# Kernel tuning notes

Hardware: AMD Instinct MI355X
Metric: run time of the kernel (lower is better)

## Reference

```python
import jax, jax.numpy as jnp
import numpy as np

# Config matching init_kwargs: dim=256, input_resolution=(64,64), num_heads=8,
# stride=2, dynamic_factor=2, window_size=8, Attention_Group=2, postype='rel', k=None
DIM, H, W = 256, 64, 64
HEADS, HG, STRIDE, WS, FACTOR = 8, 2, 2, 8, 2.0
GC = DIM // HG                 # channels per attention group (offset net width)
HC = DIM // HEADS              # per-head channels
RH, RW = H // STRIDE, W // STRIDE
WH, WW = H // WS, W // WS
B = 2
MLP_HID = 4 * DIM
EPS = 1e-5


def _grid_sample(img, grid):
    # img: (N, C, H, W); grid: (N, Hg, Wg, 2) with (row, col) in [-1, 1].
    # Bilinear, align_corners=True, zero padding (matches F.grid_sample).
    N, C, Hi, Wi = img.shape
    rows = (grid[..., 0] + 1.0) * 0.5 * (Hi - 1)
    cols = (grid[..., 1] + 1.0) * 0.5 * (Wi - 1)
    r0f = jnp.floor(rows); c0f = jnp.floor(cols)
    wr = rows - r0f; wc = cols - c0f
    r0 = r0f.astype(jnp.int32); c0 = c0f.astype(jnp.int32)

    def gather(ri, ci):
        valid = ((ri >= 0) & (ri < Hi) & (ci >= 0) & (ci < Wi)).astype(img.dtype)
        rc = jnp.clip(ri, 0, Hi - 1); cc = jnp.clip(ci, 0, Wi - 1)
        vals = jax.vmap(lambda im, r, c: im[:, r, c])(img, rc, cc)  # (N, C, Hg, Wg)
        return vals * valid[:, None]

    return (gather(r0, c0) * ((1 - wr) * (1 - wc))[:, None]
            + gather(r0, c0 + 1) * ((1 - wr) * wc)[:, None]
            + gather(r0 + 1, c0) * (wr * (1 - wc))[:, None]
            + gather(r0 + 1, c0 + 1) * (wr * wc)[:, None])


def _ln2d(z, g, b):
    mu = jnp.mean(z, axis=1, keepdims=True)
    var = jnp.var(z, axis=1, keepdims=True)
    return (z - mu) * jax.lax.rsqrt(var + EPS) * g[None, :, None, None] + b[None, :, None, None]


def _conv1x1(z, w, b=None):
    out = jnp.einsum('oc,bchw->bohw', w, z)
    return out if b is None else out + b[None, :, None, None]


def _forward(x, ln1_g, ln1_b, q_w, q_b, k_w, k_b, v_w, v_b,
             off1_w, off2_w, off3_w, bn_g, bn_b, bn_m, bn_v, off4_w,
             posembed, proj_w, proj_b, ln2_g, ln2_b,
             mlp_w1, mlp_b1, mlp_w2, mlp_b2):
    Bx, C = x.shape[0], x.shape[1]
    R, NW, WT = RH * RW, WH * WW, WS * WS
    scale = C ** -0.5  # original uses dim**-0.5 (not head_dim) as default qk scale

    xa = _ln2d(x, ln1_g, ln1_b)
    q = _conv1x1(xa, q_w, q_b)

    # ---- per-group offset prediction: 3 depthwise strided convs -> BN -> GELU -> 1x1 ----
    qg = q.reshape(Bx * HG, GC, H, W)

    def dw(z, w):
        return jax.lax.conv_general_dilated(z, w, (2, 2), ((1, 1), (1, 1)),
                feature_group_count=GC, dimension_numbers=('NCHW', 'OIHW', 'NCHW'))

    o = dw(dw(dw(qg, off1_w), off2_w), off3_w)  # (B*HG, GC, WH, WW)
    o = (o - bn_m[None, :, None, None]) * jax.lax.rsqrt(bn_v + EPS)[None, :, None, None]
    o = o * bn_g[None, :, None, None] + bn_b[None, :, None, None]
    o = jax.nn.gelu(o, approximate=False)
    off = jnp.einsum('oc,bchw->bohw', off4_w, o)               # (B*HG, 2R, WH, WW)
    off = off.reshape(Bx * HG, 2, R, NW).transpose(0, 3, 2, 1)  # (B*HG, NW, R, 2)
    ranges = jnp.array([1.0 / H, 1.0 / W], dtype=x.dtype)
    off = jnp.tanh(off) * ranges * FACTOR

    # ---- reference points normalized to [-1, 1] (align_corners=True convention) ----
    ref_r = (jnp.arange(RH, dtype=x.dtype) * STRIDE) / (H - 1) * 2.0 - 1.0
    ref_c = (jnp.arange(RW, dtype=x.dtype) * STRIDE) / (W - 1) * 2.0 - 1.0
    ref = jnp.stack(jnp.meshgrid(ref_r, ref_c, indexing='ij'), axis=-1).reshape(R, 2)
    grid = off + ref[None, None]                                # (B*HG, NW, R, 2)

    # ---- deformable gather of values at predicted sample locations ----
    value = xa.reshape(Bx * HG, GC, H, W)
    samp = _grid_sample(value, grid).reshape(Bx, C, NW, R)

    kk = _conv1x1(samp, k_w, k_b).reshape(Bx * HEADS, HC, NW, R).transpose(0, 2, 1, 3)
    vv = _conv1x1(samp, v_w, v_b).reshape(Bx * HEADS, HC, NW, R).transpose(0, 2, 1, 3)

    # ---- windowed queries ----
    wq = q.reshape(Bx * HEADS, HC, H, W).transpose(0, 2, 3, 1)
    wq = wq.reshape(Bx * HEADS, WH, WS, WW, WS, HC).transpose(0, 1, 3, 2, 4, 5)
    wq = wq.reshape(Bx * HEADS, NW, WT, HC) * scale

    attn = jnp.einsum('nwqc,nwcr->nwqr', wq, kk)                # (B*h, NW, WT, R)

    # ---- relative position bias: query pixel vs. (stride-spaced) reference point ----
    rel_y = (jnp.arange(RH) * STRIDE)[None, :] - jnp.arange(H)[:, None] + (H - 1)  # (H, RH)
    rel_x = (jnp.arange(RW) * STRIDE)[None, :] - jnp.arange(W)[:, None] + (W - 1)  # (W, RW)
    t = posembed[:, rel_y, :]                                   # (h, H, RH, 2W-1)
    bias = t[:, :, :, rel_x]                                    # (h, H, RH, W, RW)
    bias = bias.transpose(0, 1, 3, 2, 4).reshape(HEADS, H, W, R)
    bias = bias.reshape(HEADS, WH, WS, WW, WS, R).transpose(0, 1, 3, 2, 4, 5)
    bias = bias.reshape(HEADS, NW, WT, R)

    attn = attn.reshape(Bx, HEADS, NW, WT, R) + bias[None]
    attn = jax.nn.softmax(attn, axis=-1).reshape(Bx * HEADS, NW, WT, R)
    out = jnp.einsum('nwqr,nwcr->nwqc', attn, vv)               # (B*h, NW, WT, HC)
    out = out.reshape(Bx * HEADS, WH, WW, WS, WS, HC).transpose(0, 1, 3, 2, 4, 5)
    out = out.reshape(Bx, HEADS, H, W, HC).transpose(0, 1, 4, 2, 3).reshape(Bx, C, H, W)
    out = _conv1x1(out, proj_w, proj_b)

    x = x + out
    xm = _ln2d(x, ln2_g, ln2_b)
    hdn = jax.nn.gelu(_conv1x1(xm, mlp_w1, mlp_b1), approximate=False)
    return x + _conv1x1(hdn, mlp_w2, mlp_b2)


def setup_inputs() -> dict:
    key = jax.random.key(0)
    ks = jax.random.split(key, 16)
    f32 = jnp.float32

    def n(k, shape, std=0.02):
        return jax.random.normal(k, shape, dtype=f32) * std

    R = RH * RW
    return {
        'x': jax.random.normal(ks[0], (B, DIM, H, W), dtype=f32),
        'ln1_g': jnp.ones((DIM,), f32), 'ln1_b': jnp.zeros((DIM,), f32),
        'q_w': n(ks[1], (DIM, DIM)), 'q_b': jnp.zeros((DIM,), f32),
        'k_w': n(ks[2], (DIM, DIM)), 'k_b': jnp.zeros((DIM,), f32),
        'v_w': n(ks[3], (DIM, DIM)), 'v_b': jnp.zeros((DIM,), f32),
        'off1_w': n(ks[4], (GC, 1, 3, 3)),
        'off2_w': n(ks[5], (GC, 1, 3, 3)),
        'off3_w': n(ks[6], (GC, 1, 3, 3)),
        'bn_g': jnp.ones((GC,), f32), 'bn_b': jnp.zeros((GC,), f32),
        'bn_m': jnp.zeros((GC,), f32), 'bn_v': jnp.ones((GC,), f32),
        'off4_w': n(ks[7], (2 * R, GC)),
        'posembed': n(ks[8], (HEADS, 2 * H - 1, 2 * W - 1), std=0.01),
        'proj_w': n(ks[9], (DIM, DIM)), 'proj_b': jnp.zeros((DIM,), f32),
        'ln2_g': jnp.ones((DIM,), f32), 'ln2_b': jnp.zeros((DIM,), f32),
        'mlp_w1': n(ks[10], (MLP_HID, DIM)), 'mlp_b1': jnp.zeros((MLP_HID,), f32),
        'mlp_w2': n(ks[11], (DIM, MLP_HID)), 'mlp_b2': jnp.zeros((DIM,), f32),
    }


def reference(x, ln1_g, ln1_b, q_w, q_b, k_w, k_b, v_w, v_b,
              off1_w, off2_w, off3_w, bn_g, bn_b, bn_m, bn_v, off4_w,
              posembed, proj_w, proj_b, ln2_g, ln2_b,
              mlp_w1, mlp_b1, mlp_w2, mlp_b2):
    return _forward(x, ln1_g, ln1_b, q_w, q_b, k_w, k_b, v_w, v_b,
                    off1_w, off2_w, off3_w, bn_g, bn_b, bn_m, bn_v, off4_w,
                    posembed, proj_w, proj_b, ln2_g, ln2_b,
                    mlp_w1, mlp_b1, mlp_w2, mlp_b2)
```

## Files before the change

### kernel.cpp

```cpp
#include <hip/hip_runtime.h>
#include <hip/hip_bf16.h>
#include <math.h>


typedef __hip_bfloat16 bf16;
typedef __bf16 bf16x8 __attribute__((ext_vector_type(8)));
typedef float f32x4 __attribute__((ext_vector_type(4)));

union U16x8 { uint4 u4; unsigned short us[8]; };

__device__ __forceinline__ float cvt(float x) { return x; }
__device__ __forceinline__ float cvt(bf16 x) { return __bfloat162float(x); }
__device__ __forceinline__ float b2f(unsigned short u) {
  union { float f; unsigned int v; } x; x.v = ((unsigned int)u) << 16; return x.f;
}
__device__ __forceinline__ unsigned short f2b(float f) {
  bf16 h = __float2bfloat16(f);
  return *reinterpret_cast<unsigned short*>(&h);
}
__device__ __forceinline__ float gelu_f(float x) {
  return 0.5f * x * (1.0f + erff(x * 0.7071067811865475f));
}
__device__ __forceinline__ void stout(float* p, float v) { *p = v; }
__device__ __forceinline__ void stout(bf16* p, float v) { *p = __float2bfloat16(v); }

__global__ __launch_bounds__(256) void prep_kernel(
    const float* __restrict__ q_w, const float* __restrict__ q_b,
    const float* __restrict__ k_w, const float* __restrict__ v_w,
    const float* __restrict__ pjw, const float* __restrict__ w1,
    const float* __restrict__ w2, const float* __restrict__ off4w,
    unsigned short* __restrict__ wqkv, float* __restrict__ bqkv,
    unsigned short* __restrict__ wproj, unsigned short* __restrict__ wmlp1,
    unsigned short* __restrict__ wmlp2, unsigned short* __restrict__ woff4)
{
  int idx = blockIdx.x * 256 + threadIdx.x;
  const int S0 = 1280 * 256;
  const int S1 = S0 + 1280;
  const int S2 = S1 + 256 * 256;
  const int S3 = S2 + 1024 * 256;
  const int S4 = S3 + 256 * 1024;
  const int S5 = S4 + 2048 * 128;
  if (idx < S0) {
    int n = idx >> 8, c = idx & 255;
    float v;
    if (n < 256)       v = q_w[n * 256 + c];
    else if (n < 512)  v = (c < 128)  ? k_w[(n - 256) * 256 + c] : 0.f;
    else if (n < 768)  v = (c >= 128) ? k_w[(n - 512) * 256 + c] : 0.f;
    else if (n < 1024) v = (c < 128)  ? v_w[(n - 768) * 256 + c] : 0.f;
    else               v = (c >= 128) ? v_w[(n - 1024) * 256 + c] : 0.f;
    wqkv[idx] = f2b(v);
  } else if (idx < S1) {
    int n = idx - S0;
    bqkv[n] = (n < 256) ? q_b[n] : 0.f;
  } else if (idx < S2) {
    wproj[idx - S1] = f2b(pjw[idx - S1]);
  } else if (idx < S3) {
    wmlp1[idx - S2] = f2b(w1[idx - S2]);
  } else if (idx < S4) {
    wmlp2[idx - S3] = f2b(w2[idx - S3]);
  } else if (idx < S5) {
    woff4[idx - S4] = f2b(off4w[idx - S4]);
  }
}

__global__ __launch_bounds__(256) void packc_kernel(
    const float* __restrict__ rows_, const float* __restrict__ cols_,
    int* __restrict__ goff, float* __restrict__ gwt)
{
  int idx = blockIdx.x * 256 + threadIdx.x;
  float rowf = rows_[idx], colf = cols_[idx];
  float r0f = floorf(rowf), c0f = floorf(colf);
  float wr = rowf - r0f, wc = colf - c0f;
  int r0 = (int)r0f, c0 = (int)c0f;
  bool rv0 = ((unsigned)r0 < 64u), rv1 = ((unsigned)(r0 + 1) < 64u);
  bool cv0 = ((unsigned)c0 < 64u), cv1 = ((unsigned)(c0 + 1) < 64u);
  float4 w;
  w.x = (rv0 && cv0) ? (1.f - wr) * (1.f - wc) : 0.f;
  w.y = (rv0 && cv1) ? (1.f - wr) * wc : 0.f;
  w.z = (rv1 && cv0) ? wr * (1.f - wc) : 0.f;
  w.w = (rv1 && cv1) ? wr * wc : 0.f;
  goff[idx] = r0 * 64 + c0;
  *(float4*)(gwt + (size_t)idx * 4) = w;
}

__global__ __launch_bounds__(256) void ln1_kernel(
    const float* __restrict__ x, const float* __restrict__ g,
    const float* __restrict__ bta, bf16* __restrict__ out,
    float* __restrict__ xnhwc)
{
  __shared__ float s1[8][32], s2[8][32];
  __shared__ unsigned short tb[32][264];
  int t = threadIdx.x;
  int pos = t & 31, cs = t >> 5;
  int p = blockIdx.x * 32 + pos;
  int bb = p >> 12, hw = p & 4095;
  const float* xp = x + (size_t)bb * 256 * 4096 + hw;
  float vloc[32];
  float sum = 0.f, ss = 0.f;
#pragma unroll
  for (int i = 0; i < 32; ++i) {
    float v = xp[(size_t)(cs * 32 + i) * 4096];
    vloc[i] = v; sum += v; ss += v * v;
  }
  s1[cs][pos] = sum; s2[cs][pos] = ss;
  {
    float* xo = xnhwc + (size_t)p * 256 + cs * 32;
#pragma unroll
    for (int qd = 0; qd < 8; ++qd)
      *(float4*)(xo + qd * 4) = make_float4(vloc[qd*4], vloc[qd*4+1],
                                            vloc[qd*4+2], vloc[qd*4+3]);
  }
  __syncthreads();
  if (cs == 0) {
    float S = 0.f, Q = 0.f;
#pragma unroll
    for (int i = 0; i < 8; ++i) { S += s1[i][pos]; Q += s2[i][pos]; }
    float mu = S * (1.f / 256.f);
    float var = Q * (1.f / 256.f) - mu * mu;
    s1[0][pos] = mu;
    s2[0][pos] = rsqrtf(var + 1e-5f);
  }
  __syncthreads();
  float mu = s1[0][pos], rs = s2[0][pos];
#pragma unroll
  for (int i = 0; i < 32; ++i) {
    int c = cs * 32 + i;
    tb[pos][c] = f2b((vloc[i] - mu) * rs * g[c] + bta[c]);
  }
  __syncthreads();
  int px = t >> 3, grp = t & 7;
  bf16* op = out + ((size_t)blockIdx.x * 32 + px) * 256 + grp * 32;
#pragma unroll
  for (int q = 0; q < 4; ++q)
    *(uint4*)(op + q * 8) = *(const uint4*)&tb[px][grp * 32 + q * 8];
}

__global__ __launch_bounds__(256) void ln2_kernel(
    const bf16* __restrict__ xin, const float* __restrict__ g,
    const float* __restrict__ bta, bf16* __restrict__ out)
{
  __shared__ float sa[8][32], sb[8][32];
  __shared__ float mu_s[32], rs_s[32];
  int t = threadIdx.x;
  int px = t >> 3, grp = t & 7;
  size_t p = (size_t)blockIdx.x * 32 + px;
  const bf16* xp = xin + p * 256 + grp * 32;
  float v[32]; float sum = 0.f, ss = 0.f;
#pragma unroll
  for (int q = 0; q < 4; ++q) {
    U16x8 u; u.u4 = *(const uint4*)(xp + q * 8);
#pragma unroll
    for (int j = 0; j < 8; ++j) {
      float f = b2f(u.us[j]); v[q * 8 + j] = f; sum += f; ss += f * f;
    }
  }
  sa[grp][px] = sum; sb[grp][px] = ss;
  __syncthreads();
  if (t < 32) {
    float S = 0.f, Q = 0.f;
#pragma unroll
    for (int i = 0; i < 8; ++i) { S += sa[i][t]; Q += sb[i][t]; }
    float mu = S * (1.f / 256.f);
    mu_s[t] = mu;
    rs_s[t] = rsqrtf(Q * (1.f / 256.f) - mu * mu + 1e-5f);
  }
  __syncthreads();
  float mu = mu_s[px], rs = rs_s[px];
  bf16* op = out + p * 256 + grp * 32;
#pragma unroll
  for (int q = 0; q < 4; ++q) {
    U16x8 o;
#pragma unroll
    for (int j = 0; j < 8; ++j) {
      int c = grp * 32 + q * 8 + j;
      o.us[j] = f2b((v[q * 8 + j] - mu) * rs * g[c] + bta[c]);
    }
    *(uint4*)(op + q * 8) = o.u4;
  }
}

template<int OUTM, int RESM, int ACT, int BM>
__global__ __launch_bounds__(256) void mgemm_kernel(
    const bf16* __restrict__ A, const unsigned short* __restrict__ Bw,
    const float* __restrict__ bias, const void* __restrict__ res,
    void* __restrict__ out, int N, int K, int lda, int ldb)
{
  constexpr int MT = BM / 32;
// ... 23 lines not shown
      int idx = t + i * 256;
      int m = idx >> 3, oc = (idx & 7) * 8;
      *(uint4*)&As[m][oc] = *(const uint4*)(A + (size_t)(m0 + m) * lda + k0 + oc);
    }
#pragma unroll
    for (int i = 0; i < 2; ++i) {
      int idx = t + i * 256;
      int n = idx >> 3, oc = (idx & 7) * 8;
      *(uint4*)&Bs[n][oc] = *(const uint4*)(Bw + (size_t)(n0 + n) * ldb + k0 + oc);
    }
    __syncthreads();
#pragma unroll
    for (int ks = 0; ks < 2; ++ks) {
      bf16x8 af[MT], bfr[2];
#pragma unroll
      for (int mt = 0; mt < MT; ++mt)
        af[mt] = __builtin_bit_cast(bf16x8,
            *(const uint4*)&As[wm + mt * 16 + l15][ks * 32 + quad * 8]);
#pragma unroll
      for (int nt = 0; nt < 2; ++nt)
        bfr[nt] = __builtin_bit_cast(bf16x8,
            *(const uint4*)&Bs[wn + nt * 16 + l15][ks * 32 + quad * 8]);
#pragma unroll
      for (int mt = 0; mt < MT; ++mt)
#pragma unroll
        for (int nt = 0; nt < 2; ++nt)
          acc[mt][nt] = __builtin_amdgcn_mfma_f32_16x16x32_bf16(
              af[mt], bfr[nt], acc[mt][nt], 0, 0, 0);
    }
    __syncthreads();
  }
  float bv[2];
#pragma unroll
  for (int nt = 0; nt < 2; ++nt)
    bv[nt] = bias ? bias[n0 + wn + nt * 16 + l15] : 0.f;
#pragma unroll
  for (int mt = 0; mt < MT; ++mt) {
#pragma unroll
    for (int nt = 0; nt < 2; ++nt) {
#pragma unroll
      for (int reg = 0; reg < 4; ++reg) {
        int m = m0 + wm + mt * 16 + quad * 4 + reg;
        int n = n0 + wn + nt * 16 + l15;
        float v = acc[mt][nt][reg] + bv[nt];
        if constexpr (ACT == 1) v = gelu_f(v);
        if constexpr (RESM == 1)
          v += ((const float*)res)[(size_t)m * N + n];
        if constexpr (RESM == 2)
          v += b2f(((const unsigned short*)res)[(size_t)m * N + n]);
        if constexpr (OUTM == 0)
          ((unsigned short*)out)[(size_t)m * N + n] = f2b(v);
        if constexpr (OUTM == 1)
          T[(n - n0)][(m - m0)] = v;
        if constexpr (OUTM == 3) {
          float val = tanhf(v) * (2.0f / 64.0f);
          int coord = n >> 10, r = n & 1023;
          int rc = coord ? (r & 31) : (r >> 5);
          float ref = rc * (4.0f / 63.0f) - 1.0f;
          float pix = (val + ref + 1.0f) * 31.5f;
          float* dst = coord ? (float*)res : (float*)out;
          dst[(size_t)m * 1024 + r] = pix;
        }
        if constexpr (OUTM == 4)
          ((unsigned short*)out)[((size_t)(n >> 8) * 8192 + m) * 256 + (n & 255)] = f2b(v);
      }
    }
  }
  if constexpr (OUTM == 1) {
    __syncthreads();
    constexpr int SEGS = BM / 32;
    int units = 64 * SEGS;
    if (t < units) {
      int nl = t / SEGS, seg = t % SEGS;
      int bI = m0 >> 12, hw0 = m0 & 4095;
      float* op = (float*)out + ((size_t)bI * 256 + n0 + nl) * 4096 + hw0 + seg * 32;
#pragma unroll
      for (int k = 0; k < 32; ++k) op[k] = T[nl][seg * 32 + k];
    }
  }
}

template<typename TI, typename TO, int IC>
__global__ __launch_bounds__(256) void dwconv_kernel(
    const TI* __restrict__ in, const float* __restrict__ wgt,
    TO* __restrict__ out, int Hi, int Wi, int Ho, int Wo, int fuse,
    const float* __restrict__ bg_, const float* __restrict__ bb_,
    const float* __restrict__ bm_, const float* __restrict__ bv_)
{
  int idx = blockIdx.x * 256 + threadIdx.x;
  int c = idx & 127;
  int pp = idx >> 7;
  int ow = pp % Wo, oh = (pp / Wo) % Ho, bgi = pp / (Wo * Ho);
  const TI* ip;
  if constexpr (IC == 256)
    ip = in + ((size_t)(bgi >> 1) * 4096) * 256 + (bgi & 1) * 128 + c;
  else
    ip = in + ((size_t)bgi * Hi * Wi) * 128 + c;
  float acc = 0.f;
#pragma unroll
  for (int ky = 0; ky < 3; ++ky) {
    int ih = oh * 2 - 1 + ky;
    if ((unsigned)ih >= (unsigned)Hi) continue;
#pragma unroll
    for (int kx = 0; kx < 3; ++kx) {
      int iw = ow * 2 - 1 + kx;
      if ((unsigned)iw >= (unsigned)Wi) continue;
      acc += wgt[c * 9 + ky * 3 + kx] * cvt(ip[(size_t)(ih * Wi + iw) * IC]);
    }
  }
  if (fuse) {
    acc = (acc - bm_[c]) * rsqrtf(bv_[c] + 1e-5f) * bg_[c] + bb_[c];
    acc = gelu_f(acc);
  }
  stout(out + idx, acc);
}

__device__ __forceinline__ void gather_issue(
    int rc0, int b, int nw, int gr_r, int choff,
    const int* __restrict__ goff, const float* __restrict__ gwt,
    const unsigned short* __restrict__ Kimg, const unsigned short* __restrict__ Vimg,
    uint4* kc, uint4* vc, f32x4* wv)
{
#pragma unroll
  for (int g = 0; g < 2; ++g) {
    size_t cbase = ((size_t)(b * 2 + g) * 64 + nw) * 1024 + rc0 + gr_r;
    int base = goff[cbase];
    wv[g] = *(const f32x4*)(gwt + cbase * 4);
    int o00 = min(max(base, 0), 4095);
    int o01 = min(max(base + 1, 0), 4095);
    int o10 = min(max(base + 64, 0), 4095);
    int o11 = min(max(base + 65, 0), 4095);
    size_t pb = ((size_t)g * 8192 + (size_t)b * 4096) * 256 + choff;
    kc[g * 4 + 0] = *(const uint4*)(Kimg + pb + (size_t)o00 * 256);
    vc[g * 4 + 0] = *(const uint4*)(Vimg + pb + (size_t)o00 * 256);
    kc[g * 4 + 1] = *(const uint4*)(Kimg + pb + (size_t)o01 * 256);
    vc[g * 4 + 1] = *(const uint4*)(Vimg + pb + (size_t)o01 * 256);
    kc[g * 4 + 2] = *(const uint4*)(Kimg + pb + (size_t)o10 * 256);
    vc[g * 4 + 2] = *(const uint4*)(Vimg + pb + (size_t)o10 * 256);
    kc[g * 4 + 3] = *(const uint4*)(Kimg + pb + (size_t)o11 * 256);
    vc[g * 4 + 3] = *(const uint4*)(Vimg + pb + (size_t)o11 * 256);
  }
}

__global__ __launch_bounds__(256) void attn_kernel(
    const bf16* __restrict__ qbuf, const unsigned short* __restrict__ Kimg,
    const unsigned short* __restrict__ Vimg, const int* __restrict__ goff,
    const float* __restrict__ gwt, const float* __restrict__ vbv,
    const float* __restrict__ pe, bf16* __restrict__ aout)
{
  __shared__ unsigned short ks[2][64][40];
  __shared__ unsigned short vs[2][32][72];
  __shared__ unsigned short PsQs[64][72];
  __shared__ unsigned short pesb[70][72];

  int blk = blockIdx.x;
  int b = blk & 1, head = (blk >> 1) & 7, nw = blk >> 4;
  int wh = nw >> 3, ww = nw & 7;
  int t = threadIdx.x;
  int lane = t & 63, w = t >> 6;
  int l15 = lane & 15, quad = lane >> 4;
  int qc0 = head * 32;
  int gr_r = t >> 2, gr_seg = t & 3;
  int choff = qc0 + gr_seg * 8;

  {
    int qt = t >> 2, oct = t & 3;
    int h = wh * 8 + (qt >> 3), wcol = ww * 8 + (qt & 7);
// ... 119 lines not shown
        int row = gr_seg * 8 + j;
        vs[nxt][row][gr_r ^ (((row >> 3) & 3) * 8)] = f2b(aV[j]);
      }
    }
  }
#pragma unroll
  for (int nt2 = 0; nt2 < 2; ++nt2) {
    float vbias = vbv[qc0 + nt2 * 16 + l15];
#pragma unroll
    for (int reg = 0; reg < 4; ++reg) {
      int q = w * 16 + quad * 4 + reg;
      size_t p = (size_t)b * 4096 + (wh * 8 + (q >> 3)) * 64 + ww * 8 + (q & 7);
      aout[p * 256 + qc0 + nt2 * 16 + l15] =
          __float2bfloat16(oacc[nt2][reg] / l[reg] + vbias);
    }
  }
}

extern "C" void kernel_launch(void* const* d_in, const int* in_sizes, int n_in,
                              void* d_out, int out_size, void* d_ws, size_t ws_size,
                              hipStream_t stream) {
  (void)in_sizes; (void)n_in; (void)out_size; (void)ws_size;
  const float* x     = (const float*)d_in[0];
  const float* ln1g  = (const float*)d_in[1];
  const float* ln1b  = (const float*)d_in[2];
  const float* q_w   = (const float*)d_in[3];
  const float* q_b   = (const float*)d_in[4];
  const float* k_w   = (const float*)d_in[5];
  const float* k_b   = (const float*)d_in[6];
  const float* v_w   = (const float*)d_in[7];
  const float* v_b   = (const float*)d_in[8];
  const float* off1w = (const float*)d_in[9];
  const float* off2w = (const float*)d_in[10];
  const float* off3w = (const float*)d_in[11];
  const float* bng   = (const float*)d_in[12];
  const float* bnb   = (const float*)d_in[13];
  const float* bnm   = (const float*)d_in[14];
  const float* bnv   = (const float*)d_in[15];
  const float* off4w = (const float*)d_in[16];
  const float* pe    = (const float*)d_in[17];
  const float* pjw   = (const float*)d_in[18];
  const float* pjb   = (const float*)d_in[19];
  const float* ln2g  = (const float*)d_in[20];
  const float* ln2b  = (const float*)d_in[21];
  const float* w1    = (const float*)d_in[22];
  const float* b1    = (const float*)d_in[23];
  const float* w2    = (const float*)d_in[24];
  const float* b2    = (const float*)d_in[25];
  (void)k_b;
  float* outp = (float*)d_out;

  char* W = (char*)d_ws;
  bf16*  xa    = (bf16*) (W + 0);
  float* dw1   = (float*)(W + 8388608);
  float* dw2   = (float*)(W + 10485760);
  bf16*  dw3b  = (bf16*) (W + 11010048);
  float* rows  = (float*)(W + 11141120);
  float* cols  = (float*)(W + 12189696);
  bf16*  qkv   = (bf16*) (W + 13238272);
  bf16*  qb    = qkv;
  bf16*  Kimg  = qkv + 2097152;
  bf16*  Vimg  = qkv + 3 * 2097152;
  bf16*  x2    = (bf16*) (W + 34209792);
  float* xnhwc = (float*)(W + 38404096);
  unsigned short* wqkv  = (unsigned short*)(W + 46792704);
  float*          bqkv  = (float*)         (W + 47448064);
  unsigned short* wproj = (unsigned short*)(W + 47453184);
  unsigned short* wmlp1 = (unsigned short*)(W + 47584256);
  unsigned short* wmlp2 = (unsigned short*)(W + 48108544);
  unsigned short* woff4 = (unsigned short*)(W + 48632832);
  int*   goff  = (int*)  (W + 49157120);
  float* gwt   = (float*)(W + 50205696);
  bf16*  aout = xa;
  bf16*  xm   = xa;
  bf16*  hdn  = Kimg;

  prep_kernel<<<4613, 256, 0, stream>>>(q_w, q_b, k_w, v_w, pjw, w1, w2, off4w,
                                        wqkv, bqkv, wproj, wmlp1, wmlp2, woff4);
  ln1_kernel<<<256, 256, 0, stream>>>(x, ln1g, ln1b, xa, xnhwc);
  mgemm_kernel<4, 0, 0, 128><<<dim3(20, 64), 256, 0, stream>>>(
      xa, wqkv, bqkv, nullptr, qkv, 1280, 256, 256, 256);
  dwconv_kernel<bf16, float, 256><<<2048, 256, 0, stream>>>(
      qb, off1w, dw1, 64, 64, 32, 32, 0, nullptr, nullptr, nullptr, nullptr);
  dwconv_kernel<float, float, 128><<<512, 256, 0, stream>>>(
      dw1, off2w, dw2, 32, 32, 16, 16, 0, nullptr, nullptr, nullptr, nullptr);
  dwconv_kernel<float, bf16, 128><<<128, 256, 0, stream>>>(
      dw2, off3w, dw3b, 16, 16, 8, 8, 1, bng, bnb, bnm, bnv);
  mgemm_kernel<3, 0, 0, 128><<<dim3(32, 2), 256, 0, stream>>>(
      dw3b, woff4, nullptr, (const void*)cols, rows, 2048, 128, 128, 128);
  packc_kernel<<<1024, 256, 0, stream>>>(rows, cols, goff, gwt);
  attn_kernel<<<1024, 256, 0, stream>>>(
      qb, (const unsigned short*)Kimg, (const unsigned short*)Vimg,
      goff, gwt, v_b, pe, aout);
  mgemm_kernel<0, 1, 0, 64><<<dim3(4, 128), 256, 0, stream>>>(
      aout, wproj, pjb, (const void*)xnhwc, x2, 256, 256, 256, 256);
  ln2_kernel<<<256, 256, 0, stream>>>(x2, ln2g, ln2b, xm);
  mgemm_kernel<0, 0, 1, 128><<<dim3(16, 64), 256, 0, stream>>>(
      xm, wmlp1, b1, nullptr, hdn, 1024, 256, 256, 256);
  mgemm_kernel<1, 2, 0, 64><<<dim3(4, 128), 256, 0, stream>>>(
      hdn, wmlp2, b2, (const void*)x2, outp, 256, 1024, 1024, 1024);
}
```

Baseline: 316.2 us.

## Fuse dwconv chain, merge LN1 with weight prep, fold sampling-coefficient packing into GEMM

Merges the LN1 kernel and the weight-conversion kernel into one launch. Replaces the three strided depthwise conv launches with a single kernel that keeps the intermediates in shared memory, so the float intermediate buffers are no longer written and read back. Interleaves the offset-projection weight rows so row and column offsets sit in adjacent lanes, letting the GEMM epilogue compute bilinear indices and weights directly and dropping the separate packing kernel. The fused conv runs only 64 blocks with serial loops, which lowers parallelism in exchange for fewer launches and less memory traffic.

```diff
diff --git a/kernel.cpp b/kernel.cpp
--- a/kernel.cpp
+++ b/kernel.cpp
@@ -21,118 +21,98 @@
 __device__ __forceinline__ float gelu_f(float x) {
   return 0.5f * x * (1.0f + erff(x * 0.7071067811865475f));
 }
-__device__ __forceinline__ void stout(float* p, float v) { *p = v; }
-__device__ __forceinline__ void stout(bf16* p, float v) { *p = __float2bfloat16(v); }
-
-__global__ __launch_bounds__(256) void prep_kernel(
+
+__global__ __launch_bounds__(256) void setup_kernel(
+    const float* __restrict__ x, const float* __restrict__ g,
+    const float* __restrict__ bta,
     const float* __restrict__ q_w, const float* __restrict__ q_b,
     const float* __restrict__ k_w, const float* __restrict__ v_w,
     const float* __restrict__ pjw, const float* __restrict__ w1,
     const float* __restrict__ w2, const float* __restrict__ off4w,
+    bf16* __restrict__ out, float* __restrict__ xnhwc,
     unsigned short* __restrict__ wqkv, float* __restrict__ bqkv,
     unsigned short* __restrict__ wproj, unsigned short* __restrict__ wmlp1,
-    unsigned short* __restrict__ wmlp2, unsigned short* __restrict__ woff4)
-{
-  int idx = blockIdx.x * 256 + threadIdx.x;
-  const int S0 = 1280 * 256;
-  const int S1 = S0 + 1280;
-  const int S2 = S1 + 256 * 256;
-  const int S3 = S2 + 1024 * 256;
-  const int S4 = S3 + 256 * 1024;
-  const int S5 = S4 + 2048 * 128;
-  if (idx < S0) {
-    int n = idx >> 8, c = idx & 255;
-    float v;
-    if (n < 256)       v = q_w[n * 256 + c];
-    else if (n < 512)  v = (c < 128)  ? k_w[(n - 256) * 256 + c] : 0.f;
-    else if (n < 768)  v = (c >= 128) ? k_w[(n - 512) * 256 + c] : 0.f;
-    else if (n < 1024) v = (c < 128)  ? v_w[(n - 768) * 256 + c] : 0.f;
-    else               v = (c >= 128) ? v_w[(n - 1024) * 256 + c] : 0.f;
-    wqkv[idx] = f2b(v);
-  } else if (idx < S1) {
-    int n = idx - S0;
-    bqkv[n] = (n < 256) ? q_b[n] : 0.f;
-  } else if (idx < S2) {
-    wproj[idx - S1] = f2b(pjw[idx - S1]);
-  } else if (idx < S3) {
-    wmlp1[idx - S2] = f2b(w1[idx - S2]);
-  } else if (idx < S4) {
-    wmlp2[idx - S3] = f2b(w2[idx - S3]);
-  } else if (idx < S5) {
-    woff4[idx - S4] = f2b(off4w[idx - S4]);
-  }
-}
-
-__global__ __launch_bounds__(256) void packc_kernel(
-    const float* __restrict__ rows_, const float* __restrict__ cols_,
-    int* __restrict__ goff, float* __restrict__ gwt)
-{
-  int idx = blockIdx.x * 256 + threadIdx.x;
-  float rowf = rows_[idx], colf = cols_[idx];
-  float r0f = floorf(rowf), c0f = floorf(colf);
-  float wr = rowf - r0f, wc = colf - c0f;
-  int r0 = (int)r0f, c0 = (int)c0f;
-  bool rv0 = ((unsigned)r0 < 64u), rv1 = ((unsigned)(r0 + 1) < 64u);
-  bool cv0 = ((unsigned)c0 < 64u), cv1 = ((unsigned)(c0 + 1) < 64u);
-  float4 w;
-  w.x = (rv0 && cv0) ? (1.f - wr) * (1.f - wc) : 0.f;
-  w.y = (rv0 && cv1) ? (1.f - wr) * wc : 0.f;
-  w.z = (rv1 && cv0) ? wr * (1.f - wc) : 0.f;
-  w.w = (rv1 && cv1) ? wr * wc : 0.f;
-  goff[idx] = r0 * 64 + c0;
-  *(float4*)(gwt + (size_t)idx * 4) = w;
-}
-
-__global__ __launch_bounds__(256) void ln1_kernel(
-    const float* __restrict__ x, const float* __restrict__ g,
-    const float* __restrict__ bta, bf16* __restrict__ out,
-    float* __restrict__ xnhwc)
+    unsigned short* __restrict__ wmlp2, unsigned short* __restrict__ woff4i)
 {
   __shared__ float s1[8][32], s2[8][32];
   __shared__ unsigned short tb[32][264];
+  int bid = blockIdx.x;
   int t = threadIdx.x;
-  int pos = t & 31, cs = t >> 5;
-  int p = blockIdx.x * 32 + pos;
-  int bb = p >> 12, hw = p & 4095;
-  const float* xp = x + (size_t)bb * 256 * 4096 + hw;
-  float vloc[32];
-  float sum = 0.f, ss = 0.f;
-#pragma unroll
-  for (int i = 0; i < 32; ++i) {
-    float v = xp[(size_t)(cs * 32 + i) * 4096];
-    vloc[i] = v; sum += v; ss += v * v;
-  }
-  s1[cs][pos] = sum; s2[cs][pos] = ss;
-  {
-    float* xo = xnhwc + (size_t)p * 256 + cs * 32;
-#pragma unroll
-    for (int qd = 0; qd < 8; ++qd)
-      *(float4*)(xo + qd * 4) = make_float4(vloc[qd*4], vloc[qd*4+1],
-                                            vloc[qd*4+2], vloc[qd*4+3]);
-  }
-  __syncthreads();
-  if (cs == 0) {
-    float S = 0.f, Q = 0.f;
-#pragma unroll
-    for (int i = 0; i < 8; ++i) { S += s1[i][pos]; Q += s2[i][pos]; }
-    float mu = S * (1.f / 256.f);
-    float var = Q * (1.f / 256.f) - mu * mu;
-    s1[0][pos] = mu;
-    s2[0][pos] = rsqrtf(var + 1e-5f);
-  }
-  __syncthreads();
-  float mu = s1[0][pos], rs = s2[0][pos];
-#pragma unroll
-  for (int i = 0; i < 32; ++i) {
-    int c = cs * 32 + i;
-    tb[pos][c] = f2b((vloc[i] - mu) * rs * g[c] + bta[c]);
-  }
-  __syncthreads();
-  int px = t >> 3, grp = t & 7;
-  bf16* op = out + ((size_t)blockIdx.x * 32 + px) * 256 + grp * 32;
-#pragma unroll
-  for (int q = 0; q < 4; ++q)
-    *(uint4*)(op + q * 8) = *(const uint4*)&tb[px][grp * 32 + q * 8];
+  if (bid < 256) {
+    int pos = t & 31, cs = t >> 5;
+    int p = bid * 32 + pos;
+    int bb = p >> 12, hw = p & 4095;
+    const float* xp = x + (size_t)bb * 256 * 4096 + hw;
+    float vloc[32];
+    float sum = 0.f, ss = 0.f;
+#pragma unroll
+    for (int i = 0; i < 32; ++i) {
+      float v = xp[(size_t)(cs * 32 + i) * 4096];
+      vloc[i] = v; sum += v; ss += v * v;
+    }
+    s1[cs][pos] = sum; s2[cs][pos] = ss;
+    {
+      float* xo = xnhwc + (size_t)p * 256 + cs * 32;
+#pragma unroll
+      for (int qd = 0; qd < 8; ++qd)
+        *(float4*)(xo + qd * 4) = make_float4(vloc[qd*4], vloc[qd*4+1],
+                                              vloc[qd*4+2], vloc[qd*4+3]);
+    }
+    __syncthreads();
+    if (cs == 0) {
+      float S = 0.f, Q = 0.f;
+#pragma unroll
+      for (int i = 0; i < 8; ++i) { S += s1[i][pos]; Q += s2[i][pos]; }
+      float mu = S * (1.f / 256.f);
+      float var = Q * (1.f / 256.f) - mu * mu;
+      s1[0][pos] = mu;
+      s2[0][pos] = rsqrtf(var + 1e-5f);
+    }
+    __syncthreads();
+    float mu = s1[0][pos], rs = s2[0][pos];
+#pragma unroll
+    for (int i = 0; i < 32; ++i) {
+      int c = cs * 32 + i;
+      tb[pos][c] = f2b((vloc[i] - mu) * rs * g[c] + bta[c]);
+    }
+    __syncthreads();
+    int px = t >> 3, grp = t & 7;
+    bf16* op = out + ((size_t)bid * 32 + px) * 256 + grp * 32;
+#pragma unroll
+    for (int q = 0; q < 4; ++q)
+      *(uint4*)(op + q * 8) = *(const uint4*)&tb[px][grp * 32 + q * 8];
+  } else {
+    int idx = (bid - 256) * 256 + t;
+    const int S0 = 1280 * 256;
+    const int S1 = S0 + 1280;
+    const int S2 = S1 + 256 * 256;
+    const int S3 = S2 + 1024 * 256;
+    const int S4 = S3 + 256 * 1024;
+    const int S5 = S4 + 2048 * 128;
+    if (idx < S0) {
+      int n = idx >> 8, c = idx & 255;
+      float v;
+      if (n < 256)       v = q_w[n * 256 + c];
+      else if (n < 512)  v = (c < 128)  ? k_w[(n - 256) * 256 + c] : 0.f;
+      else if (n < 768)  v = (c >= 128) ? k_w[(n - 512) * 256 + c] : 0.f;
+      else if (n < 1024) v = (c < 128)  ? v_w[(n - 768) * 256 + c] : 0.f;
+      else               v = (c >= 128) ? v_w[(n - 1024) * 256 + c] : 0.f;
+      wqkv[idx] = f2b(v);
+    } else if (idx < S1) {
+      int n = idx - S0;
+      bqkv[n] = (n < 256) ? q_b[n] : 0.f;
+    } else if (idx < S2) {
+      wproj[idx - S1] = f2b(pjw[idx - S1]);
+    } else if (idx < S3) {
+      wmlp1[idx - S2] = f2b(w1[idx - S2]);
+    } else if (idx < S4) {
+      wmlp2[idx - S3] = f2b(w2[idx - S3]);
+    } else if (idx < S5) {
+      int kk = idx - S4;
+      int n = kk >> 7, c = kk & 127;
+      woff4i[kk] = f2b(off4w[((size_t)((n & 1) * 1024 + (n >> 1))) * 128 + c]);
+    }
+  }
 }
 
 __global__ __launch_bounds__(256) void ln2_kernel(
@@ -262,17 +242,31 @@
           ((unsigned short*)out)[(size_t)m * N + n] = f2b(v);
         if constexpr (OUTM == 1)
           T[(n - n0)][(m - m0)] = v;
-        if constexpr (OUTM == 3) {
+        if constexpr (OUTM == 4)
+          ((unsigned short*)out)[((size_t)(n >> 8) * 8192 + m) * 256 + (n & 255)] = f2b(v);
+        if constexpr (OUTM == 5) {
           float val = tanhf(v) * (2.0f / 64.0f);
-          int coord = n >> 10, r = n & 1023;
+          int r = n >> 1, coord = n & 1;
           int rc = coord ? (r & 31) : (r >> 5);
           float ref = rc * (4.0f / 63.0f) - 1.0f;
           float pix = (val + ref + 1.0f) * 31.5f;
-          float* dst = coord ? (float*)res : (float*)out;
-          dst[(size_t)m * 1024 + r] = pix;
+          float other = __shfl_xor(pix, 1, 64);
+          if (coord == 0) {
+            float rowp = pix, colp = other;
+            float r0f = floorf(rowp), c0f = floorf(colp);
+            float wr = rowp - r0f, wc = colp - c0f;
+            int r0 = (int)r0f, c0 = (int)c0f;
+            bool rv0 = ((unsigned)r0 < 64u), rv1 = ((unsigned)(r0 + 1) < 64u);
+            bool cv0 = ((unsigned)c0 < 64u), cv1 = ((unsigned)(c0 + 1) < 64u);
+            float4 w4;
+            w4.x = (rv0 && cv0) ? (1.f - wr) * (1.f - wc) : 0.f;
+            w4.y = (rv0 && cv1) ? (1.f - wr) * wc : 0.f;
+            w4.z = (rv1 && cv0) ? wr * (1.f - wc) : 0.f;
+            w4.w = (rv1 && cv1) ? wr * wc : 0.f;
+            ((int*)out)[(size_t)m * 1024 + r] = r0 * 64 + c0;
+            *(float4*)((float*)res + ((size_t)m * 1024 + r) * 4) = w4;
+          }
         }
-        if constexpr (OUTM == 4)
-          ((unsigned short*)out)[((size_t)(n >> 8) * 8192 + m) * 256 + (n & 255)] = f2b(v);
       }
     }
   }
@@ -290,39 +284,87 @@
   }
 }
 
-template<typename TI, typename TO, int IC>
-__global__ __launch_bounds__(256) void dwconv_kernel(
-    const TI* __restrict__ in, const float* __restrict__ wgt,
-    TO* __restrict__ out, int Hi, int Wi, int Ho, int Wo, int fuse,
-    const float* __restrict__ bg_, const float* __restrict__ bb_,
-    const float* __restrict__ bm_, const float* __restrict__ bv_)
+__global__ __launch_bounds__(256) void dwfused_kernel(
+    const bf16* __restrict__ qb, const float* __restrict__ w1_,
+    const float* __restrict__ w2_, const float* __restrict__ w3_,
+    const float* __restrict__ bng, const float* __restrict__ bnb,
+    const float* __restrict__ bnm, const float* __restrict__ bnv,
+    bf16* __restrict__ dw3b)
 {
-  int idx = blockIdx.x * 256 + threadIdx.x;
-  int c = idx & 127;
-  int pp = idx >> 7;
-  int ow = pp % Wo, oh = (pp / Wo) % Ho, bgi = pp / (Wo * Ho);
-  const TI* ip;
-  if constexpr (IC == 256)
-    ip = in + ((size_t)(bgi >> 1) * 4096) * 256 + (bgi & 1) * 128 + c;
-  else
-    ip = in + ((size_t)bgi * Hi * Wi) * 128 + c;
-  float acc = 0.f;
-#pragma unroll
-  for (int ky = 0; ky < 3; ++ky) {
-    int ih = oh * 2 - 1 + ky;
-    if ((unsigned)ih >= (unsigned)Hi) continue;
-#pragma unroll
-    for (int kx = 0; kx < 3; ++kx) {
-      int iw = ow * 2 - 1 + kx;
-      if ((unsigned)iw >= (unsigned)Wi) continue;
-      acc += wgt[c * 9 + ky * 3 + kx] * cvt(ip[(size_t)(ih * Wi + iw) * IC]);
-    }
-  }
-  if (fuse) {
-    acc = (acc - bm_[c]) * rsqrtf(bv_[c] + 1e-5f) * bg_[c] + bb_[c];
+  __shared__ float L1[1024][8];
+  __shared__ float L2[256][8];
+  int blk = blockIdx.x;
+  int bg = blk >> 4, cg = blk & 15;
+  int b = bg >> 1, g = bg & 1;
+  int t = threadIdx.x;
+  int cl = t & 7;
+  int c127 = cg * 8 + cl;
+  int choff = g * 128 + c127;
+  float wreg[9];
+#pragma unroll
+  for (int k = 0; k < 9; ++k) wreg[k] = w1_[c127 * 9 + k];
+  for (int i = 0; i < 32; ++i) {
+    int sp = (t >> 3) + i * 32;
+    int oh = sp >> 5, ow = sp & 31;
+    float acc = 0.f;
+#pragma unroll
+    for (int ky = 0; ky < 3; ++ky) {
+      int ih = oh * 2 - 1 + ky;
+      if ((unsigned)ih >= 64u) continue;
+#pragma unroll
+      for (int kx = 0; kx < 3; ++kx) {
+        int iw = ow * 2 - 1 + kx;
+        if ((unsigned)iw >= 64u) continue;
+        acc += wreg[ky * 3 + kx] *
+               cvt(qb[((size_t)b * 4096 + ih * 64 + iw) * 256 + choff]);
+      }
+    }
+    L1[sp][cl] = acc;
+  }
+  __syncthreads();
+#pragma unroll
+  for (int k = 0; k < 9; ++k) wreg[k] = w2_[c127 * 9 + k];
+  for (int i = 0; i < 8; ++i) {
+    int sp = (t >> 3) + i * 32;
+    int oh = sp >> 4, ow = sp & 15;
+    float acc = 0.f;
+#pragma unroll
+    for (int ky = 0; ky < 3; ++ky) {
+      int ih = oh * 2 - 1 + ky;
+      if ((unsigned)ih >= 32u) continue;
+#pragma unroll
+      for (int kx = 0; kx < 3; ++kx) {
+        int iw = ow * 2 - 1 + kx;
+        if ((unsigned)iw >= 32u) continue;
+        acc += wreg[ky * 3 + kx] * L1[ih * 32 + iw][cl];
+      }
+    }
+    L2[sp][cl] = acc;
+  }
+  __syncthreads();
+#pragma unroll
+  for (int k = 0; k < 9; ++k) wreg[k] = w3_[c127 * 9 + k];
+  float sc = rsqrtf(bnv[c127] + 1e-5f) * bng[c127];
+  float mb = bnm[c127], bb2 = bnb[c127];
+  for (int i = 0; i < 2; ++i) {
+    int sp = (t >> 3) + i * 32;
+    int oh = sp >> 3, ow = sp & 7;
+    float acc = 0.f;
+#pragma unroll
+    for (int ky = 0; ky < 3; ++ky) {
+      int ih = oh * 2 - 1 + ky;
+      if ((unsigned)ih >= 16u) continue;
+#pragma unroll
+      for (int kx = 0; kx < 3; ++kx) {
+        int iw = ow * 2 - 1 + kx;
+        if ((unsigned)iw >= 16u) continue;
+        acc += wreg[ky * 3 + kx] * L2[ih * 16 + iw][cl];
+      }
+    }
+    acc = (acc - mb) * sc + bb2;
     acc = gelu_f(acc);
-  }
-  stout(out + idx, acc);
+    dw3b[((size_t)bg * 64 + sp) * 128 + c127] = __float2bfloat16(acc);
+  }
 }
 
 __device__ __forceinline__ void gather_issue(
@@ -548,43 +590,34 @@
 
   char* W = (char*)d_ws;
   bf16*  xa    = (bf16*) (W + 0);
-  float* dw1   = (float*)(W + 8388608);
-  float* dw2   = (float*)(W + 10485760);
   bf16*  dw3b  = (bf16*) (W + 11010048);
-  float* rows  = (float*)(W + 11141120);
-  float* cols  = (float*)(W + 12189696);
   bf16*  qkv   = (bf16*) (W + 13238272);
   bf16*  qb    = qkv;
   bf16*  Kimg  = qkv + 2097152;
   bf16*  Vimg  = qkv + 3 * 2097152;
   bf16*  x2    = (bf16*) (W + 34209792);
   float* xnhwc = (float*)(W + 38404096);
-  unsigned short* wqkv  = (unsigned short*)(W + 46792704);
-  float*          bqkv  = (float*)         (W + 47448064);
-  unsigned short* wproj = (unsigned short*)(W + 47453184);
-  unsigned short* wmlp1 = (unsigned short*)(W + 47584256);
-  unsigned short* wmlp2 = (unsigned short*)(W + 48108544);
-  unsigned short* woff4 = (unsigned short*)(W + 48632832);
+  unsigned short* wqkv   = (unsigned short*)(W + 46792704);
+  float*          bqkv   = (float*)         (W + 47448064);
+  unsigned short* wproj  = (unsigned short*)(W + 47453184);
+  unsigned short* wmlp1  = (unsigned short*)(W + 47584256);
+  unsigned short* wmlp2  = (unsigned short*)(W + 48108544);
+  unsigned short* woff4i = (unsigned short*)(W + 48632832);
   int*   goff  = (int*)  (W + 49157120);
   float* gwt   = (float*)(W + 50205696);
   bf16*  aout = xa;
   bf16*  xm   = xa;
   bf16*  hdn  = Kimg;
 
-  prep_kernel<<<4613, 256, 0, stream>>>(q_w, q_b, k_w, v_w, pjw, w1, w2, off4w,
-                                        wqkv, bqkv, wproj, wmlp1, wmlp2, woff4);
-  ln1_kernel<<<256, 256, 0, stream>>>(x, ln1g, ln1b, xa, xnhwc);
+  setup_kernel<<<4869, 256, 0, stream>>>(
+      x, ln1g, ln1b, q_w, q_b, k_w, v_w, pjw, w1, w2, off4w,
+      xa, xnhwc, wqkv, bqkv, wproj, wmlp1, wmlp2, woff4i);
   mgemm_kernel<4, 0, 0, 128><<<dim3(20, 64), 256, 0, stream>>>(
       xa, wqkv, bqkv, nullptr, qkv, 1280, 256, 256, 256);
-  dwconv_kernel<bf16, float, 256><<<2048, 256, 0, stream>>>(
-      qb, off1w, dw1, 64, 64, 32, 32, 0, nullptr, nullptr, nullptr, nullptr);
-  dwconv_kernel<float, float, 128><<<512, 256, 0, stream>>>(
-      dw1, off2w, dw2, 32, 32, 16, 16, 0, nullptr, nullptr, nullptr, nullptr);
-  dwconv_kernel<float, bf16, 128><<<128, 256, 0, stream>>>(
-      dw2, off3w, dw3b, 16, 16, 8, 8, 1, bng, bnb, bnm, bnv);
-  mgemm_kernel<3, 0, 0, 128><<<dim3(32, 2), 256, 0, stream>>>(
-      dw3b, woff4, nullptr, (const void*)cols, rows, 2048, 128, 128, 128);
-  packc_kernel<<<1024, 256, 0, stream>>>(rows, cols, goff, gwt);
+  dwfused_kernel<<<64, 256, 0, stream>>>(qb, off1w, off2w, off3w,
+                                         bng, bnb, bnm, bnv, dw3b);
+  mgemm_kernel<5, 0, 0, 128><<<dim3(32, 2), 256, 0, stream>>>(
+      dw3b, woff4i, nullptr, (const void*)gwt, goff, 2048, 128, 128, 128);
   attn_kernel<<<1024, 256, 0, stream>>>(
       qb, (const unsigned short*)Kimg, (const unsigned short*)Vimg,
       goff, gwt, v_b, pe, aout);
```

Measured after the change: 352.7 us. +11.5%, slower.

## Fuse LN1 with weight prep and fold bilinear packing into offset GEMM epilogue

Applied to the files above, without the earlier changes.

Merges the weight-conversion kernel and the LN1 kernel into one launch by splitting the grid on block index. It also interleaves the offset-projection weight rows so row and column coordinates land in adjacent lanes. A lane shuffle then lets the offset GEMM epilogue compute the bilinear gather offsets and weights directly, so the packc kernel and the rows/cols intermediates go away. This cuts two launches and a round trip through global memory, at the cost of a more complex epilogue and reliance on lane pairing.

```diff
diff --git a/kernel.cpp b/kernel.cpp
--- a/kernel.cpp
+++ b/kernel.cpp
@@ -24,115 +24,97 @@
 __device__ __forceinline__ void stout(float* p, float v) { *p = v; }
 __device__ __forceinline__ void stout(bf16* p, float v) { *p = __float2bfloat16(v); }
 
-__global__ __launch_bounds__(256) void prep_kernel(
+__global__ __launch_bounds__(256) void setup_kernel(
+    const float* __restrict__ x, const float* __restrict__ g,
+    const float* __restrict__ bta,
     const float* __restrict__ q_w, const float* __restrict__ q_b,
     const float* __restrict__ k_w, const float* __restrict__ v_w,
     const float* __restrict__ pjw, const float* __restrict__ w1,
     const float* __restrict__ w2, const float* __restrict__ off4w,
+    bf16* __restrict__ out, float* __restrict__ xnhwc,
     unsigned short* __restrict__ wqkv, float* __restrict__ bqkv,
     unsigned short* __restrict__ wproj, unsigned short* __restrict__ wmlp1,
-    unsigned short* __restrict__ wmlp2, unsigned short* __restrict__ woff4)
-{
-  int idx = blockIdx.x * 256 + threadIdx.x;
-  const int S0 = 1280 * 256;
-  const int S1 = S0 + 1280;
-  const int S2 = S1 + 256 * 256;
-  const int S3 = S2 + 1024 * 256;
-  const int S4 = S3 + 256 * 1024;
-  const int S5 = S4 + 2048 * 128;
-  if (idx < S0) {
-    int n = idx >> 8, c = idx & 255;
-    float v;
-    if (n < 256)       v = q_w[n * 256 + c];
-    else if (n < 512)  v = (c < 128)  ? k_w[(n - 256) * 256 + c] : 0.f;
-    else if (n < 768)  v = (c >= 128) ? k_w[(n - 512) * 256 + c] : 0.f;
-    else if (n < 1024) v = (c < 128)  ? v_w[(n - 768) * 256 + c] : 0.f;
-    else               v = (c >= 128) ? v_w[(n - 1024) * 256 + c] : 0.f;
-    wqkv[idx] = f2b(v);
-  } else if (idx < S1) {
-    int n = idx - S0;
-    bqkv[n] = (n < 256) ? q_b[n] : 0.f;
-  } else if (idx < S2) {
-    wproj[idx - S1] = f2b(pjw[idx - S1]);
-  } else if (idx < S3) {
-    wmlp1[idx - S2] = f2b(w1[idx - S2]);
-  } else if (idx < S4) {
-    wmlp2[idx - S3] = f2b(w2[idx - S3]);
-  } else if (idx < S5) {
-    woff4[idx - S4] = f2b(off4w[idx - S4]);
-  }
-}
-
-__global__ __launch_bounds__(256) void packc_kernel(
-    const float* __restrict__ rows_, const float* __restrict__ cols_,
-    int* __restrict__ goff, float* __restrict__ gwt)
-{
-  int idx = blockIdx.x * 256 + threadIdx.x;
-  float rowf = rows_[idx], colf = cols_[idx];
-  float r0f = floorf(rowf), c0f = floorf(colf);
-  float wr = rowf - r0f, wc = colf - c0f;
-  int r0 = (int)r0f, c0 = (int)c0f;
-  bool rv0 = ((unsigned)r0 < 64u), rv1 = ((unsigned)(r0 + 1) < 64u);
-  bool cv0 = ((unsigned)c0 < 64u), cv1 = ((unsigned)(c0 + 1) < 64u);
-  float4 w;
-  w.x = (rv0 && cv0) ? (1.f - wr) * (1.f - wc) : 0.f;
-  w.y = (rv0 && cv1) ? (1.f - wr) * wc : 0.f;
-  w.z = (rv1 && cv0) ? wr * (1.f - wc) : 0.f;
-  w.w = (rv1 && cv1) ? wr * wc : 0.f;
-  goff[idx] = r0 * 64 + c0;
-  *(float4*)(gwt + (size_t)idx * 4) = w;
-}
-
-__global__ __launch_bounds__(256) void ln1_kernel(
-    const float* __restrict__ x, const float* __restrict__ g,
-    const float* __restrict__ bta, bf16* __restrict__ out,
-    float* __restrict__ xnhwc)
+    unsigned short* __restrict__ wmlp2, unsigned short* __restrict__ woff4i)
 {
   __shared__ float s1[8][32], s2[8][32];
   __shared__ unsigned short tb[32][264];
+  int bid = blockIdx.x;
   int t = threadIdx.x;
-  int pos = t & 31, cs = t >> 5;
-  int p = blockIdx.x * 32 + pos;
-  int bb = p >> 12, hw = p & 4095;
-  const float* xp = x + (size_t)bb * 256 * 4096 + hw;
-  float vloc[32];
-  float sum = 0.f, ss = 0.f;
-#pragma unroll
-  for (int i = 0; i < 32; ++i) {
-    float v = xp[(size_t)(cs * 32 + i) * 4096];
-    vloc[i] = v; sum += v; ss += v * v;
-  }
-  s1[cs][pos] = sum; s2[cs][pos] = ss;
-  {
-    float* xo = xnhwc + (size_t)p * 256 + cs * 32;
-#pragma unroll
-    for (int qd = 0; qd < 8; ++qd)
-      *(float4*)(xo + qd * 4) = make_float4(vloc[qd*4], vloc[qd*4+1],
-                                            vloc[qd*4+2], vloc[qd*4+3]);
-  }
-  __syncthreads();
-  if (cs == 0) {
-    float S = 0.f, Q = 0.f;
-#pragma unroll
-    for (int i = 0; i < 8; ++i) { S += s1[i][pos]; Q += s2[i][pos]; }
-    float mu = S * (1.f / 256.f);
-    float var = Q * (1.f / 256.f) - mu * mu;
-    s1[0][pos] = mu;
-    s2[0][pos] = rsqrtf(var + 1e-5f);
-  }
-  __syncthreads();
-  float mu = s1[0][pos], rs = s2[0][pos];
-#pragma unroll
-  for (int i = 0; i < 32; ++i) {
-    int c = cs * 32 + i;
-    tb[pos][c] = f2b((vloc[i] - mu) * rs * g[c] + bta[c]);
-  }
-  __syncthreads();
-  int px = t >> 3, grp = t & 7;
-  bf16* op = out + ((size_t)blockIdx.x * 32 + px) * 256 + grp * 32;
-#pragma unroll
-  for (int q = 0; q < 4; ++q)
-    *(uint4*)(op + q * 8) = *(const uint4*)&tb[px][grp * 32 + q * 8];
+  if (bid < 256) {
+    int pos = t & 31, cs = t >> 5;
+    int p = bid * 32 + pos;
+    int bb = p >> 12, hw = p & 4095;
+    const float* xp = x + (size_t)bb * 256 * 4096 + hw;
+    float vloc[32];
+    float sum = 0.f, ss = 0.f;
+#pragma unroll
+    for (int i = 0; i < 32; ++i) {
+      float v = xp[(size_t)(cs * 32 + i) * 4096];
+      vloc[i] = v; sum += v; ss += v * v;
+    }
+    s1[cs][pos] = sum; s2[cs][pos] = ss;
+    {
+      float* xo = xnhwc + (size_t)p * 256 + cs * 32;
+#pragma unroll
+      for (int qd = 0; qd < 8; ++qd)
+        *(float4*)(xo + qd * 4) = make_float4(vloc[qd*4], vloc[qd*4+1],
+                                              vloc[qd*4+2], vloc[qd*4+3]);
+    }
+    __syncthreads();
+    if (cs == 0) {
+      float S = 0.f, Q = 0.f;
+#pragma unroll
+      for (int i = 0; i < 8; ++i) { S += s1[i][pos]; Q += s2[i][pos]; }
+      float mu = S * (1.f / 256.f);
+      float var = Q * (1.f / 256.f) - mu * mu;
+      s1[0][pos] = mu;
+      s2[0][pos] = rsqrtf(var + 1e-5f);
+    }
+    __syncthreads();
+    float mu = s1[0][pos], rs = s2[0][pos];
+#pragma unroll
+    for (int i = 0; i < 32; ++i) {
+      int c = cs * 32 + i;
+      tb[pos][c] = f2b((vloc[i] - mu) * rs * g[c] + bta[c]);
+    }
+    __syncthreads();
+    int px = t >> 3, grp = t & 7;
+    bf16* op = out + ((size_t)bid * 32 + px) * 256 + grp * 32;
+#pragma unroll
+    for (int q = 0; q < 4; ++q)
+      *(uint4*)(op + q * 8) = *(const uint4*)&tb[px][grp * 32 + q * 8];
+  } else {
+    int idx = (bid - 256) * 256 + t;
+    const int S0 = 1280 * 256;
+    const int S1 = S0 + 1280;
+    const int S2 = S1 + 256 * 256;
+    const int S3 = S2 + 1024 * 256;
+    const int S4 = S3 + 256 * 1024;
+    const int S5 = S4 + 2048 * 128;
+    if (idx < S0) {
+      int n = idx >> 8, c = idx & 255;
+      float v;
+      if (n < 256)       v = q_w[n * 256 + c];
+      else if (n < 512)  v = (c < 128)  ? k_w[(n - 256) * 256 + c] : 0.f;
+      else if (n < 768)  v = (c >= 128) ? k_w[(n - 512) * 256 + c] : 0.f;
+      else if (n < 1024) v = (c < 128)  ? v_w[(n - 768) * 256 + c] : 0.f;
+      else               v = (c >= 128) ? v_w[(n - 1024) * 256 + c] : 0.f;
+      wqkv[idx] = f2b(v);
+    } else if (idx < S1) {
+      int n = idx - S0;
+      bqkv[n] = (n < 256) ? q_b[n] : 0.f;
+    } else if (idx < S2) {
+      wproj[idx - S1] = f2b(pjw[idx - S1]);
+    } else if (idx < S3) {
+      wmlp1[idx - S2] = f2b(w1[idx - S2]);
+    } else if (idx < S4) {
+      wmlp2[idx - S3] = f2b(w2[idx - S3]);
+    } else if (idx < S5) {
+      int kk = idx - S4;
+      int n = kk >> 7, c = kk & 127;
+      woff4i[kk] = f2b(off4w[((size_t)((n & 1) * 1024 + (n >> 1))) * 128 + c]);
+    }
+  }
 }
 
 __global__ __launch_bounds__(256) void ln2_kernel(
@@ -262,17 +244,31 @@
           ((unsigned short*)out)[(size_t)m * N + n] = f2b(v);
         if constexpr (OUTM == 1)
           T[(n - n0)][(m - m0)] = v;
-        if constexpr (OUTM == 3) {
+        if constexpr (OUTM == 4)
+          ((unsigned short*)out)[((size_t)(n >> 8) * 8192 + m) * 256 + (n & 255)] = f2b(v);
+        if constexpr (OUTM == 5) {
           float val = tanhf(v) * (2.0f / 64.0f);
-          int coord = n >> 10, r = n & 1023;
+          int r = n >> 1, coord = n & 1;
           int rc = coord ? (r & 31) : (r >> 5);
           float ref = rc * (4.0f / 63.0f) - 1.0f;
           float pix = (val + ref + 1.0f) * 31.5f;
-          float* dst = coord ? (float*)res : (float*)out;
-          dst[(size_t)m * 1024 + r] = pix;
+          float other = __shfl_xor(pix, 1, 64);
+          if (coord == 0) {
+            float rowp = pix, colp = other;
+            float r0f = floorf(rowp), c0f = floorf(colp);
+            float wr = rowp - r0f, wc = colp - c0f;
+            int r0 = (int)r0f, c0 = (int)c0f;
+            bool rv0 = ((unsigned)r0 < 64u), rv1 = ((unsigned)(r0 + 1) < 64u);
+            bool cv0 = ((unsigned)c0 < 64u), cv1 = ((unsigned)(c0 + 1) < 64u);
+            float4 w4;
+            w4.x = (rv0 && cv0) ? (1.f - wr) * (1.f - wc) : 0.f;
+            w4.y = (rv0 && cv1) ? (1.f - wr) * wc : 0.f;
+            w4.z = (rv1 && cv0) ? wr * (1.f - wc) : 0.f;
+            w4.w = (rv1 && cv1) ? wr * wc : 0.f;
+            ((int*)out)[(size_t)m * 1024 + r] = r0 * 64 + c0;
+            *(float4*)((float*)res + ((size_t)m * 1024 + r) * 4) = w4;
+          }
         }
-        if constexpr (OUTM == 4)
-          ((unsigned short*)out)[((size_t)(n >> 8) * 8192 + m) * 256 + (n & 255)] = f2b(v);
       }
     }
   }
@@ -551,29 +547,27 @@
   float* dw1   = (float*)(W + 8388608);
   float* dw2   = (float*)(W + 10485760);
   bf16*  dw3b  = (bf16*) (W + 11010048);
-  float* rows  = (float*)(W + 11141120);
-  float* cols  = (float*)(W + 12189696);
   bf16*  qkv   = (bf16*) (W + 13238272);
   bf16*  qb    = qkv;
   bf16*  Kimg  = qkv + 2097152;
   bf16*  Vimg  = qkv + 3 * 2097152;
   bf16*  x2    = (bf16*) (W + 34209792);
   float* xnhwc = (float*)(W + 38404096);
-  unsigned short* wqkv  = (unsigned short*)(W + 46792704);
-  float*          bqkv  = (float*)         (W + 47448064);
-  unsigned short* wproj = (unsigned short*)(W + 47453184);
-  unsigned short* wmlp1 = (unsigned short*)(W + 47584256);
-  unsigned short* wmlp2 = (unsigned short*)(W + 48108544);
-  unsigned short* woff4 = (unsigned short*)(W + 48632832);
+  unsigned short* wqkv   = (unsigned short*)(W + 46792704);
+  float*          bqkv   = (float*)         (W + 47448064);
+  unsigned short* wproj  = (unsigned short*)(W + 47453184);
+  unsigned short* wmlp1  = (unsigned short*)(W + 47584256);
+  unsigned short* wmlp2  = (unsigned short*)(W + 48108544);
+  unsigned short* woff4i = (unsigned short*)(W + 48632832);
   int*   goff  = (int*)  (W + 49157120);
   float* gwt   = (float*)(W + 50205696);
   bf16*  aout = xa;
   bf16*  xm   = xa;
   bf16*  hdn  = Kimg;
 
-  prep_kernel<<<4613, 256, 0, stream>>>(q_w, q_b, k_w, v_w, pjw, w1, w2, off4w,
-                                        wqkv, bqkv, wproj, wmlp1, wmlp2, woff4);
-  ln1_kernel<<<256, 256, 0, stream>>>(x, ln1g, ln1b, xa, xnhwc);
+  setup_kernel<<<4869, 256, 0, stream>>>(
+      x, ln1g, ln1b, q_w, q_b, k_w, v_w, pjw, w1, w2, off4w,
+      xa, xnhwc, wqkv, bqkv, wproj, wmlp1, wmlp2, woff4i);
   mgemm_kernel<4, 0, 0, 128><<<dim3(20, 64), 256, 0, stream>>>(
       xa, wqkv, bqkv, nullptr, qkv, 1280, 256, 256, 256);
   dwconv_kernel<bf16, float, 256><<<2048, 256, 0, stream>>>(
@@ -582,9 +576,8 @@
       dw1, off2w, dw2, 32, 32, 16, 16, 0, nullptr, nullptr, nullptr, nullptr);
   dwconv_kernel<float, bf16, 128><<<128, 256, 0, stream>>>(
       dw2, off3w, dw3b, 16, 16, 8, 8, 1, bng, bnb, bnm, bnv);
-  mgemm_kernel<3, 0, 0, 128><<<dim3(32, 2), 256, 0, stream>>>(
-      dw3b, woff4, nullptr, (const void*)cols, rows, 2048, 128, 128, 128);
-  packc_kernel<<<1024, 256, 0, stream>>>(rows, cols, goff, gwt);
+  mgemm_kernel<5, 0, 0, 128><<<dim3(32, 2), 256, 0, stream>>>(
+      dw3b, woff4i, nullptr, (const void*)gwt, goff, 2048, 128, 128, 128);
   attn_kernel<<<1024, 256, 0, stream>>>(
       qb, (const unsigned short*)Kimg, (const unsigned short*)Vimg,
       goff, gwt, v_b, pe, aout);
```

Result: no change. 313.3 us (-0.9%).
